# Kernel tuning notes

Hardware: AMD Instinct MI355X
Metric: run time of the kernel (lower is better)

The kernel has to match this reference:

```python
import jax, jax.numpy as jnp
import numpy as np

N_NODES = 100000


def gcn_conv(x, W, b, row, col, n):
    """PyG GCNConv: linear transform, then symmetric-normalized aggregation
    with self-loops (add_self_loops=True, normalize=True, bias=True)."""
    h = x @ W  # [N, F_out]
    e_ones = jnp.ones(row.shape[0], dtype=x.dtype)
    # in-degree of target nodes, +1 for the implicit self-loop
    deg = jax.ops.segment_sum(e_ones, col, num_segments=n) + 1.0
    dinv = jax.lax.rsqrt(deg)  # deg >= 1 always
    norm = dinv[row] * dinv[col]  # [E]
    msg = h[row] * norm[:, None]  # gather + scale, [E, F_out]
    agg = jax.ops.segment_sum(msg, col, num_segments=n)  # scatter-add to targets
    agg = agg + h * (dinv * dinv)[:, None]  # self-loop contribution
    return agg + b


def setup_inputs() -> dict:
    key = jax.random.key(0)
    k1, k2, k3, k4 = jax.random.split(key, 4)
    F_in, F_hid, F_out = 512, 64, 40
    E = 1_600_000
    x = jax.random.normal(k1, (N_NODES, F_in), dtype=jnp.float32)
    edge_index = jax.random.randint(k2, (2, E), 0, N_NODES, dtype=jnp.int64)
    # Glorot-ish scaling for weights
    W1 = jax.random.normal(k3, (F_in, F_hid), dtype=jnp.float32) * (1.0 / np.sqrt(F_in))
    W2 = jax.random.normal(k4, (F_hid, F_out), dtype=jnp.float32) * (1.0 / np.sqrt(F_hid))
    b1 = jnp.zeros((F_hid,), dtype=jnp.float32)
    b2 = jnp.zeros((F_out,), dtype=jnp.float32)
    return {"x": x, "edge_index": edge_index, "W1": W1, "b1": b1, "W2": W2, "b2": b2}


def reference(x, edge_index, W1, b1, W2, b2):
    n = x.shape[0]
    row, col = edge_index[0], edge_index[1]
    h = jax.nn.relu(gcn_conv(x, W1, b1, row, col, n))
    # dropout is identity in eval mode (training=False)
    h = gcn_conv(h, W2, b2, row, col, n)
    return jax.nn.log_softmax(h, axis=1)
```

## Files before the change

kernel.cpp:

```cpp
#include <hip/hip_runtime.h>
#include <math.h>


#define FIN 512
#define FHID 64
#define FOUT 40

#define BSH 8
#define BN 256
#define BCAP 5120
#define EPW 4096

typedef __attribute__((ext_vector_type(8))) short short8;
typedef __attribute__((ext_vector_type(4))) float f32x4;
typedef __attribute__((ext_vector_type(4))) float float4v;
typedef unsigned short ushort_t;
typedef unsigned int uint_t;
typedef __attribute__((ext_vector_type(4))) uint_t uint4v;

__device__ __forceinline__ ushort_t bf16_rn(float f) {
    union { float f; uint_t u; } v; v.f = f;
    uint_t r = v.u + 0x7FFF + ((v.u >> 16) & 1);
    return (ushort_t)(r >> 16);
}
__device__ __forceinline__ uint_t pack_bf16(float a, float b) {
    return (uint_t)bf16_rn(a) | ((uint_t)bf16_rn(b) << 16);
}
__device__ __forceinline__ float bf16_to_f(ushort_t u) {
    union { uint_t i; float f; } t; t.i = ((uint_t)u) << 16; return t.f;
}
__device__ __forceinline__ void add8(float* acc, uint4 g) {
    acc[0] += __uint_as_float(g.x << 16);
    acc[1] += __uint_as_float(g.x & 0xFFFF0000u);
    acc[2] += __uint_as_float(g.y << 16);
    acc[3] += __uint_as_float(g.y & 0xFFFF0000u);
    acc[4] += __uint_as_float(g.z << 16);
    acc[5] += __uint_as_float(g.z & 0xFFFF0000u);
    acc[6] += __uint_as_float(g.w << 16);
    acc[7] += __uint_as_float(g.w & 0xFFFF0000u);
}

__global__ void wprep_kernel(const float* __restrict__ W1, const float* __restrict__ W2,
                             ushort_t* __restrict__ Wt,
                             ushort_t* __restrict__ w2hi, ushort_t* __restrict__ w2lo,
                             int* __restrict__ gcur,
                             ushort_t* __restrict__ sent1, ushort_t* __restrict__ sent2) {
    int idx = blockIdx.x * 256 + threadIdx.x;
    if (idx < 512) gcur[idx] = 0;
    if (idx < 64) { sent1[idx] = 0; sent2[idx] = 0; }
    if (idx < 32768) {
        int nrow = idx >> 9;
        int k = idx & 511;
        Wt[idx] = bf16_rn(W1[k * 64 + nrow]);
    } else if (idx < 32768 + 3072) {
        int i = idx - 32768;
        int j = i >> 6, k = i & 63;
        float w = (j < FOUT) ? W2[k * FOUT + j] : 0.f;
        ushort_t h = bf16_rn(w);
        w2hi[i] = h;
        w2lo[i] = bf16_rn(w - bf16_to_f(h));
    }
}

__global__ __launch_bounds__(256) void bucket_scatter_kernel(
    const int* __restrict__ row, const int* __restrict__ col,
    int* __restrict__ gcur, uint_t* __restrict__ stage, int E) {
    __shared__ uint_t cnt[512];
    __shared__ uint_t base[512];
    int tid = threadIdx.x;
    cnt[tid] = 0; cnt[tid + 256] = 0;
    __syncthreads();
    int e0 = blockIdx.x * EPW;
    int creg[16];
#pragma unroll
    for (int it = 0; it < 16; ++it) {
        int e = e0 + it * 256 + tid;
        creg[it] = (e < E) ? __builtin_nontemporal_load(&col[e]) : -1;
        if (e < E) atomicAdd(&cnt[((uint_t)creg[it]) >> BSH], 1u);
    }
    __syncthreads();
    uint_t c0 = cnt[tid], c1 = cnt[tid + 256];
    base[tid] = c0 ? (uint_t)atomicAdd(&gcur[tid], (int)c0) : 0u;
    base[tid + 256] = c1 ? (uint_t)atomicAdd(&gcur[tid + 256], (int)c1) : 0u;
    __syncthreads();
    cnt[tid] = 0; cnt[tid + 256] = 0;
    __syncthreads();
#pragma unroll
    for (int it = 0; it < 16; ++it) {
        int e = e0 + it * 256 + tid;
        if (e < E) {
            int c = creg[it];
            int r = __builtin_nontemporal_load(&row[e]);
            int b = c >> BSH;
            uint_t slot = base[b] + atomicAdd(&cnt[b], 1u);
            stage[(size_t)b * BCAP + slot] = ((uint_t)r << BSH) | (uint_t)(c & (BN - 1));
        }
    }
}

__global__ __launch_bounds__(256) void bucket_place_kernel(
    const int* __restrict__ gcur, const uint_t* __restrict__ stage,
    int* __restrict__ sSrc, int* __restrict__ deg, float* __restrict__ dinv,
    int* __restrict__ offs, int n) {
    __shared__ int sc[512];
    __shared__ int lcnt[256];
    __shared__ int ltmp[256];
    __shared__ int lpos[256];
    int b = blockIdx.x, tid = threadIdx.x;
    int i1 = tid + 256;
    sc[tid] = gcur[tid];
    sc[i1] = gcur[i1];
    __syncthreads();
    for (int off = 1; off < 512; off <<= 1) {
        int a0 = (tid >= off) ? sc[tid - off] : 0;
        int a1 = (i1 >= off) ? sc[i1 - off] : 0;
        __syncthreads();
        sc[tid] += a0; sc[i1] += a1;
        __syncthreads();
    }
    int cntB = gcur[b];
    int bucketBase = sc[b] - cntB;
    int nodeBase = b << BSH;
    lcnt[tid] = 0;
    __syncthreads();
    const uint_t* sp = &stage[(size_t)b * BCAP];
    for (int i = tid; i < cntB; i += 256)
        atomicAdd(&lcnt[__builtin_nontemporal_load(&sp[i]) & (BN - 1)], 1);
    __syncthreads();
    int v = lcnt[tid];
    ltmp[tid] = v;
    __syncthreads();
    for (int off = 1; off < 256; off <<= 1) {
        int t = (tid >= off) ? ltmp[tid - off] : 0;
        __syncthreads();
        ltmp[tid] += t;
        __syncthreads();
    }
    int gofs = bucketBase + ltmp[tid] - v;
    int node = nodeBase + tid;
    if (node < n) {
        deg[node] = v;
        dinv[node] = rsqrtf((float)v + 1.0f);
        offs[node] = gofs;
    }
    lpos[tid] = gofs;
    __syncthreads();
    for (int i = tid; i < cntB; i += 256) {
        uint_t w = __builtin_nontemporal_load(&sp[i]);
        int pos = atomicAdd(&lpos[w & (BN - 1)], 1);
        sSrc[pos] = (int)(w >> BSH);
    }
}

#define LDA 72
#define LDB 72
__global__ __launch_bounds__(256) void gemm1_kernel(
    const float* __restrict__ x, const ushort_t* __restrict__ Wt,
    const float* __restrict__ dinv, ushort_t* __restrict__ h1b, int n) {
    __shared__ ushort_t lA[128 * LDA];
    __shared__ ushort_t lB[64 * LDB];

    int tid = threadIdx.x;
    int wave = tid >> 6, lane = tid & 63;
    int quad = lane >> 4, m16 = lane & 15;
    int node0 = blockIdx.x * 128;

    int r0 = tid >> 4, k4 = tid & 15;
    int nr0 = tid >> 3, seg = tid & 7;

    f32x4 zero = {0.f, 0.f, 0.f, 0.f};
    f32x4 acc[2][4];
#pragma unroll
    for (int mt = 0; mt < 2; ++mt)
#pragma unroll
        for (int nt = 0; nt < 4; ++nt) acc[mt][nt] = zero;

    float4v ra[8];
    uint4 rb[2];

#pragma unroll
    for (int i = 0; i < 8; ++i) {
        int node = node0 + r0 + i * 16;
        float4v v = {0.f, 0.f, 0.f, 0.f};
        if (node < n)
            v = __builtin_nontemporal_load(
                reinterpret_cast<const float4v*>(&x[(size_t)node * FIN + k4 * 4]));
        ra[i] = v;
    }
#pragma unroll
    for (int i = 0; i < 2; ++i)
        rb[i] = *reinterpret_cast<const uint4*>(&Wt[(size_t)(nr0 + i * 32) * FIN + seg * 8]);

    for (int c = 0; c < 8; ++c) {
#pragma unroll
        for (int i = 0; i < 8; ++i)
            *reinterpret_cast<uint2*>(&lA[(r0 + i * 16) * LDA + k4 * 4]) =
                make_uint2(pack_bf16(ra[i][0], ra[i][1]), pack_bf16(ra[i][2], ra[i][3]));
#pragma unroll
        for (int i = 0; i < 2; ++i)
            *reinterpret_cast<uint4*>(&lB[(nr0 + i * 32) * LDB + seg * 8]) = rb[i];
        __syncthreads();

        if (c < 7) {
            int kc = (c + 1) * 64;
#pragma unroll
            for (int i = 0; i < 8; ++i) {
                int node = node0 + r0 + i * 16;
                float4v v = {0.f, 0.f, 0.f, 0.f};
                if (node < n)
                    v = __builtin_nontemporal_load(
                        reinterpret_cast<const float4v*>(&x[(size_t)node * FIN + kc + k4 * 4]));
                ra[i] = v;
            }
#pragma unroll
            for (int i = 0; i < 2; ++i)
                rb[i] = *reinterpret_cast<const uint4*>(
                    &Wt[(size_t)(nr0 + i * 32) * FIN + kc + seg * 8]);
        }

#pragma unroll
        for (int kk = 0; kk < 2; ++kk) {
            short8 a[2], b[4];
#pragma unroll
            for (int mt = 0; mt < 2; ++mt)
                a[mt] = *reinterpret_cast<const short8*>(
                    &lA[(wave * 32 + mt * 16 + m16) * LDA + kk * 32 + quad * 8]);
#pragma unroll
            for (int nt = 0; nt < 4; ++nt)
                b[nt] = *reinterpret_cast<const short8*>(
                    &lB[(nt * 16 + m16) * LDB + kk * 32 + quad * 8]);
#pragma unroll
            for (int mt = 0; mt < 2; ++mt)
#pragma unroll
                for (int nt = 0; nt < 4; ++nt)
                    acc[mt][nt] = __builtin_amdgcn_mfma_f32_16x16x32_bf16(
                        a[mt], b[nt], acc[mt][nt], 0, 0, 0);
        }
        __syncthreads();
    }

#pragma unroll
    for (int mt = 0; mt < 2; ++mt) {
#pragma unroll
        for (int reg = 0; reg < 4; ++reg) {
            int node = node0 + wave * 32 + mt * 16 + quad * 4 + reg;
            if (node < n) {
                float di = dinv[node];
#pragma unroll
                for (int nt = 0; nt < 4; ++nt)
                    h1b[(size_t)node * 64 + nt * 16 + m16] =
                        bf16_rn(acc[mt][nt][reg] * di);
            }
        }
    }
}

template <int MODE>
__global__ __launch_bounds__(256) void agg_kernel(
    const int* __restrict__ offs, const int* __restrict__ deg,
    const int* __restrict__ sSrc, const ushort_t* __restrict__ src,
    const float* __restrict__ dinv, const float* __restrict__ b1,
    ushort_t* __restrict__ dst, int n) {
    __shared__ float lacc[8][4 * 68];
    __shared__ float lb1[64];
    int tid = threadIdx.x;
    if (MODE == 0 && tid < 64) lb1[tid] = b1[tid];

    int wv = tid >> 6, lane = tid & 63;
    int half = lane >> 5;
    int l32 = lane & 31;
    int e4 = l32 >> 3, c = l32 & 7;
    int slot = wv * 2 + half;
    int node = blockIdx.x * 8 + slot;
    bool valid = node < n;
    int start = valid ? offs[node] : 0;
    int cnt = valid ? deg[node] : 0;

    float acc[8];
#pragma unroll
    for (int j = 0; j < 8; ++j) acc[j] = 0.f;

    for (int base = 0; base < cnt; base += 16) {
        int i0 = base + e4, i1 = i0 + 4, i2 = i0 + 8, i3 = i0 + 12;
        int s0 = (i0 < cnt) ? __builtin_nontemporal_load(&sSrc[start + i0]) : n;
        int s1 = (i1 < cnt) ? __builtin_nontemporal_load(&sSrc[start + i1]) : n;
        int s2 = (i2 < cnt) ? __builtin_nontemporal_load(&sSrc[start + i2]) : n;
        int s3 = (i3 < cnt) ? __builtin_nontemporal_load(&sSrc[start + i3]) : n;
        uint4 g0 = *reinterpret_cast<const uint4*>(&src[(size_t)s0 * 64 + c * 8]);
        uint4 g1 = *reinterpret_cast<const uint4*>(&src[(size_t)s1 * 64 + c * 8]);
        uint4 g2 = *reinterpret_cast<const uint4*>(&src[(size_t)s2 * 64 + c * 8]);
        uint4 g3 = *reinterpret_cast<const uint4*>(&src[(size_t)s3 * 64 + c * 8]);
        add8(acc, g0);
        add8(acc, g1);
        add8(acc, g2);
        add8(acc, g3);
    }

    {
        float* lw = &lacc[slot][e4 * 68 + c * 8];
        *reinterpret_cast<float4*>(lw) = make_float4(acc[0], acc[1], acc[2], acc[3]);
        *reinterpret_cast<float4*>(lw + 4) = make_float4(acc[4], acc[5], acc[6], acc[7]);
    }
    __syncthreads();

    int s = tid >> 5;
    int fp = tid & 31;
    int enode = blockIdx.x * 8 + s;
    if (enode < n) {
        float sum0 = 0.f, sum1 = 0.f;
#pragma unroll
        for (int g = 0; g < 4; ++g) {
            sum0 += lacc[s][g * 68 + fp * 2];
            sum1 += lacc[s][g * 68 + fp * 2 + 1];
        }
        float di = dinv[enode];
        uint_t sv = *reinterpret_cast<const uint_t*>(&src[(size_t)enode * 64 + fp * 2]);
        float self0 = __uint_as_float(sv << 16);
        float self1 = __uint_as_float(sv & 0xFFFF0000u);
        float v0 = (sum0 + self0) * di;
        float v1 = (sum1 + self1) * di;
        if (MODE == 0) {
            v0 = fmaxf(v0 + lb1[fp * 2], 0.f) * di;
            v1 = fmaxf(v1 + lb1[fp * 2 + 1], 0.f) * di;
        }
        *reinterpret_cast<uint_t*>(&dst[(size_t)enode * 64 + fp * 2]) = pack_bf16(v0, v1);
    }
}

#define LDC 72
__global__ __launch_bounds__(256) void gemm2sm_kernel(
    const ushort_t* __restrict__ A, const ushort_t* __restrict__ w2hi,
    const ushort_t* __restrict__ w2lo, const float* __restrict__ b2,
    float* __restrict__ out, int n) {
    __shared__ ushort_t lA[128 * LDC];
    __shared__ ushort_t lBh[48 * LDC];
    __shared__ ushort_t lBl[48 * LDC];

    int tid = threadIdx.x;
    int wave = tid >> 6, lane = tid & 63;
    int quad = lane >> 4, m16 = lane & 15;
    int node0 = blockIdx.x * 128;

    {
        int r = tid & 127, part = tid >> 7;
        int node = node0 + r;
        uint4v z = {0u, 0u, 0u, 0u};
        const uint4v* sp = reinterpret_cast<const uint4v*>(&A[(size_t)node * 64 + part * 32]);
#pragma unroll
        for (int i = 0; i < 4; ++i) {
            uint4v v = (node < n) ? __builtin_nontemporal_load(sp + i) : z;
            *reinterpret_cast<uint4v*>(&lA[r * LDC + part * 32 + i * 8]) = v;
        }
    }
    for (int i = tid; i < 384; i += 256) {
        int row = i >> 3, seg = i & 7;
        *reinterpret_cast<uint4*>(&lBh[row * LDC + seg * 8]) =
            reinterpret_cast<const uint4*>(w2hi)[i];
        *reinterpret_cast<uint4*>(&lBl[row * LDC + seg * 8]) =
            reinterpret_cast<const uint4*>(w2lo)[i];
    }
    float rb2_0 = b2[m16];
    float rb2_1 = b2[16 + m16];
    float rb2_2 = (m16 < 8) ? b2[32 + m16] : 0.f;
    __syncthreads();

    f32x4 zero = {0.f, 0.f, 0.f, 0.f};
    f32x4 acc[2][3];
#pragma unroll
    for (int mt = 0; mt < 2; ++mt)
#pragma unroll
        for (int nt = 0; nt < 3; ++nt) acc[mt][nt] = zero;

#pragma unroll
    for (int kk = 0; kk < 2; ++kk) {
        short8 a[2], bh[3], bl[3];
#pragma unroll
        for (int mt = 0; mt < 2; ++mt)
            a[mt] = *reinterpret_cast<const short8*>(
                &lA[(wave * 32 + mt * 16 + m16) * LDC + kk * 32 + quad * 8]);
#pragma unroll
        for (int nt = 0; nt < 3; ++nt) {
            bh[nt] = *reinterpret_cast<const short8*>(
                &lBh[(nt * 16 + m16) * LDC + kk * 32 + quad * 8]);
            bl[nt] = *reinterpret_cast<const short8*>(
                &lBl[(nt * 16 + m16) * LDC + kk * 32 + quad * 8]);
        }
#pragma unroll
        for (int mt = 0; mt < 2; ++mt)
#pragma unroll
            for (int nt = 0; nt < 3; ++nt) {
                acc[mt][nt] = __builtin_amdgcn_mfma_f32_16x16x32_bf16(
                    a[mt], bh[nt], acc[mt][nt], 0, 0, 0);
                acc[mt][nt] = __builtin_amdgcn_mfma_f32_16x16x32_bf16(
                    a[mt], bl[nt], acc[mt][nt], 0, 0, 0);
            }
    }

    bool c2 = (m16 < 8);
#pragma unroll
    for (int mt = 0; mt < 2; ++mt) {
#pragma unroll
        for (int reg = 0; reg < 4; ++reg) {
            int node = node0 + wave * 32 + mt * 16 + quad * 4 + reg;
            float r0 = acc[mt][0][reg] + rb2_0;
            float r1 = acc[mt][1][reg] + rb2_1;
            float r2 = acc[mt][2][reg] + rb2_2;
            float pm = fmaxf(fmaxf(r0, r1), c2 ? r2 : -INFINITY);
#pragma unroll
            for (int mask = 1; mask <= 8; mask <<= 1)
                pm = fmaxf(pm, __shfl_xor(pm, mask));
            float s = expf(r0 - pm) + expf(r1 - pm) + (c2 ? expf(r2 - pm) : 0.f);
#pragma unroll
            for (int mask = 1; mask <= 8; mask <<= 1)
                s += __shfl_xor(s, mask);
            float ls = logf(s) + pm;
            if (node < n) {
                float* op = &out[(size_t)node * FOUT];
                __builtin_nontemporal_store(r0 - ls, &op[m16]);
                __builtin_nontemporal_store(r1 - ls, &op[16 + m16]);
                if (c2) __builtin_nontemporal_store(r2 - ls, &op[32 + m16]);
            }
        }
    }
}

extern "C" void kernel_launch(void* const* d_in, const int* in_sizes, int n_in,
                              void* d_out, int out_size, void* d_ws, size_t ws_size,
                              hipStream_t stream) {
    const float* x  = (const float*)d_in[0];
    const int*   ei = (const int*)d_in[1];
    const float* W1 = (const float*)d_in[2];
    const float* b1 = (const float*)d_in[3];
    const float* W2 = (const float*)d_in[4];
    const float* b2 = (const float*)d_in[5];
    float* out = (float*)d_out;

    int n = in_sizes[0] / FIN;
    int E = in_sizes[1] / 2;
    const int* row = ei;
    const int* col = ei + E;

    int* wsi = (int*)d_ws;
    const size_t NR = 100352;
    int*      deg   = wsi;
    float*    dinv  = (float*)(wsi + NR);
    int*      offs  = wsi + 2 * NR;
    int*      gcur  = wsi + 3 * NR;
    ushort_t* Wt    = (ushort_t*)(wsi + 3 * NR + 512);
    ushort_t* w2hi  = Wt + 64 * 512;
    ushort_t* w2lo  = w2hi + 48 * 64;
    uint_t*   stage = (uint_t*)(w2lo + 48 * 64);
    int*      sSrc  = (int*)(stage + (size_t)512 * BCAP);
    ushort_t* h1b   = (ushort_t*)(sSrc + (size_t)E);
    ushort_t* h1a   = h1b + (size_t)(n + 1) * 64;
    ushort_t* Abuf  = h1b;

    int NBUCK = (n + BN - 1) >> BSH;
    int nwg1 = (E + EPW - 1) / EPW;

    wprep_kernel<<<140, 256, 0, stream>>>(W1, W2, Wt, w2hi, w2lo, gcur,
                                          h1b + (size_t)n * 64, h1a + (size_t)n * 64);

    bucket_scatter_kernel<<<nwg1, 256, 0, stream>>>(row, col, gcur, stage, E);
    bucket_place_kernel<<<NBUCK, 256, 0, stream>>>(gcur, stage, sSrc, deg, dinv, offs, n);

    gemm1_kernel<<<(n + 127) / 128, 256, 0, stream>>>(x, Wt, dinv, h1b, n);

    agg_kernel<0><<<(n + 7) / 8, 256, 0, stream>>>(offs, deg, sSrc, h1b, dinv, b1, h1a, n);

    agg_kernel<1><<<(n + 7) / 8, 256, 0, stream>>>(offs, deg, sSrc, h1a, dinv, b1, Abuf, n);

    gemm2sm_kernel<<<(n + 127) / 128, 256, 0, stream>>>(Abuf, w2hi, w2lo, b2, out, n);
}
```

Before: 432.1 us.

## Fuse second-layer aggregation into GEMM2 kernel via LDS staging

The second GCN aggregation is moved into the GEMM2 kernel. Each 128-node block gathers neighbor features for its nodes in 16 iterations and writes the normalized result straight into the LDS A-tile, instead of round-tripping through a global buffer. This removes one kernel launch and a full intermediate write and read. In exchange, the aggregation now runs with far fewer blocks and more serial work per block, which reduces latency hiding for the irregular gathers. The first aggregation kernel is specialized to drop the template mode.

```diff
diff --git a/kernel.cpp b/kernel.cpp
--- a/kernel.cpp
+++ b/kernel.cpp
@@ -255,8 +255,7 @@
     }
 }
 
-template <int MODE>
-__global__ __launch_bounds__(256) void agg_kernel(
+__global__ __launch_bounds__(256) void agg1_kernel(
     const int* __restrict__ offs, const int* __restrict__ deg,
     const int* __restrict__ sSrc, const ushort_t* __restrict__ src,
     const float* __restrict__ dinv, const float* __restrict__ b1,
@@ -264,7 +263,7 @@
     __shared__ float lacc[8][4 * 68];
     __shared__ float lb1[64];
     int tid = threadIdx.x;
-    if (MODE == 0 && tid < 64) lb1[tid] = b1[tid];
+    if (tid < 64) lb1[tid] = b1[tid];
 
     int wv = tid >> 6, lane = tid & 63;
     int half = lane >> 5;
@@ -317,41 +316,29 @@
         uint_t sv = *reinterpret_cast<const uint_t*>(&src[(size_t)enode * 64 + fp * 2]);
         float self0 = __uint_as_float(sv << 16);
         float self1 = __uint_as_float(sv & 0xFFFF0000u);
-        float v0 = (sum0 + self0) * di;
-        float v1 = (sum1 + self1) * di;
-        if (MODE == 0) {
-            v0 = fmaxf(v0 + lb1[fp * 2], 0.f) * di;
-            v1 = fmaxf(v1 + lb1[fp * 2 + 1], 0.f) * di;
-        }
+        float v0 = fmaxf((sum0 + self0) * di + lb1[fp * 2], 0.f) * di;
+        float v1 = fmaxf((sum1 + self1) * di + lb1[fp * 2 + 1], 0.f) * di;
         *reinterpret_cast<uint_t*>(&dst[(size_t)enode * 64 + fp * 2]) = pack_bf16(v0, v1);
     }
 }
 
 #define LDC 72
-__global__ __launch_bounds__(256) void gemm2sm_kernel(
-    const ushort_t* __restrict__ A, const ushort_t* __restrict__ w2hi,
+__global__ __launch_bounds__(256) void agg2gemm2sm_kernel(
+    const int* __restrict__ offs, const int* __restrict__ deg,
+    const int* __restrict__ sSrc, const ushort_t* __restrict__ src,
+    const float* __restrict__ dinv, const ushort_t* __restrict__ w2hi,
     const ushort_t* __restrict__ w2lo, const float* __restrict__ b2,
     float* __restrict__ out, int n) {
     __shared__ ushort_t lA[128 * LDC];
     __shared__ ushort_t lBh[48 * LDC];
     __shared__ ushort_t lBl[48 * LDC];
+    __shared__ float lacc[8][4 * 68];
 
     int tid = threadIdx.x;
     int wave = tid >> 6, lane = tid & 63;
     int quad = lane >> 4, m16 = lane & 15;
     int node0 = blockIdx.x * 128;
 
-    {
-        int r = tid & 127, part = tid >> 7;
-        int node = node0 + r;
-        uint4v z = {0u, 0u, 0u, 0u};
-        const uint4v* sp = reinterpret_cast<const uint4v*>(&A[(size_t)node * 64 + part * 32]);
-#pragma unroll
-        for (int i = 0; i < 4; ++i) {
-            uint4v v = (node < n) ? __builtin_nontemporal_load(sp + i) : z;
-            *reinterpret_cast<uint4v*>(&lA[r * LDC + part * 32 + i * 8]) = v;
-        }
-    }
     for (int i = tid; i < 384; i += 256) {
         int row = i >> 3, seg = i & 7;
         *reinterpret_cast<uint4*>(&lBh[row * LDC + seg * 8]) =
@@ -362,6 +349,59 @@
     float rb2_0 = b2[m16];
     float rb2_1 = b2[16 + m16];
     float rb2_2 = (m16 < 8) ? b2[32 + m16] : 0.f;
+
+    int half = lane >> 5;
+    int l32 = lane & 31;
+    int e4 = l32 >> 3, c = l32 & 7;
+    int slot = wave * 2 + half;
+    int fp = l32;
+
+    for (int it = 0; it < 16; ++it) {
+        int node = node0 + it * 8 + slot;
+        bool valid = node < n;
+        int start = valid ? offs[node] : 0;
+        int cnt = valid ? deg[node] : 0;
+
+        float acc[8];
+#pragma unroll
+        for (int j = 0; j < 8; ++j) acc[j] = 0.f;
+
+        for (int base = 0; base < cnt; base += 16) {
+            int i0 = base + e4, i1 = i0 + 4, i2 = i0 + 8, i3 = i0 + 12;
+            int s0 = (i0 < cnt) ? __builtin_nontemporal_load(&sSrc[start + i0]) : n;
+            int s1 = (i1 < cnt) ? __builtin_nontemporal_load(&sSrc[start + i1]) : n;
+            int s2 = (i2 < cnt) ? __builtin_nontemporal_load(&sSrc[start + i2]) : n;
+            int s3 = (i3 < cnt) ? __builtin_nontemporal_load(&sSrc[start + i3]) : n;
+            uint4 g0 = *reinterpret_cast<const uint4*>(&src[(size_t)s0 * 64 + c * 8]);
+            uint4 g1 = *reinterpret_cast<const uint4*>(&src[(size_t)s1 * 64 + c * 8]);
+            uint4 g2 = *reinterpret_cast<const uint4*>(&src[(size_t)s2 * 64 + c * 8]);
+            uint4 g3 = *reinterpret_cast<const uint4*>(&src[(size_t)s3 * 64 + c * 8]);
+            add8(acc, g0);
+            add8(acc, g1);
+            add8(acc, g2);
+            add8(acc, g3);
+        }
+
+        {
+            float* lw = &lacc[slot][e4 * 68 + c * 8];
+            *reinterpret_cast<float4*>(lw) = make_float4(acc[0], acc[1], acc[2], acc[3]);
+            *reinterpret_cast<float4*>(lw + 4) = make_float4(acc[4], acc[5], acc[6], acc[7]);
+        }
+        float sum0 = 0.f, sum1 = 0.f;
+#pragma unroll
+        for (int g = 0; g < 4; ++g) {
+            sum0 += lacc[slot][g * 68 + fp * 2];
+            sum1 += lacc[slot][g * 68 + fp * 2 + 1];
+        }
+        float v0 = 0.f, v1 = 0.f;
+        if (node < n) {
+            float di = dinv[node];
+            uint_t sv = *reinterpret_cast<const uint_t*>(&src[(size_t)node * 64 + fp * 2]);
+            v0 = (sum0 + __uint_as_float(sv << 16)) * di;
+            v1 = (sum1 + __uint_as_float(sv & 0xFFFF0000u)) * di;
+        }
+        *reinterpret_cast<uint_t*>(&lA[(it * 8 + slot) * LDC + fp * 2]) = pack_bf16(v0, v1);
+    }
     __syncthreads();
 
     f32x4 zero = {0.f, 0.f, 0.f, 0.f};
@@ -453,7 +493,6 @@
     int*      sSrc  = (int*)(stage + (size_t)512 * BCAP);
     ushort_t* h1b   = (ushort_t*)(sSrc + (size_t)E);
     ushort_t* h1a   = h1b + (size_t)(n + 1) * 64;
-    ushort_t* Abuf  = h1b;
 
     int NBUCK = (n + BN - 1) >> BSH;
     int nwg1 = (E + EPW - 1) / EPW;
@@ -466,9 +505,8 @@
 
     gemm1_kernel<<<(n + 127) / 128, 256, 0, stream>>>(x, Wt, dinv, h1b, n);
 
-    agg_kernel<0><<<(n + 7) / 8, 256, 0, stream>>>(offs, deg, sSrc, h1b, dinv, b1, h1a, n);
-
-    agg_kernel<1><<<(n + 7) / 8, 256, 0, stream>>>(offs, deg, sSrc, h1a, dinv, b1, Abuf, n);
-
-    gemm2sm_kernel<<<(n + 127) / 128, 256, 0, stream>>>(Abuf, w2hi, w2lo, b2, out, n);
-}
+    agg1_kernel<<<(n + 7) / 8, 256, 0, stream>>>(offs, deg, sSrc, h1b, dinv, b1, h1a, n);
+
+    agg2gemm2sm_kernel<<<(n + 127) / 128, 256, 0, stream>>>(
+        offs, deg, sSrc, h1a, dinv, w2hi, w2lo, b2, out, n);
+}
```

Result: no change. 439.4 us (+1.7%).
